# Kernel optimization log

Measured on AMD Instinct MI355X. Metric: run time of the kernel, lower is better.

Reference implementation:

```python
import jax, jax.numpy as jnp
import numpy as np

EMBED_DIM = 1024
NUM_HEADS = 16
HEAD_DIM = EMBED_DIM // NUM_HEADS
B, T = 8, 1024


def setup_inputs() -> dict:
    key = jax.random.key(0)
    ks = jax.random.split(key, 8)
    s = EMBED_DIM ** -0.5
    return {
        "query": jax.random.normal(ks[0], (B, T, EMBED_DIM), jnp.float32),
        "key": jax.random.normal(ks[1], (B, T, EMBED_DIM), jnp.float32),
        "value": jax.random.normal(ks[2], (B, T, EMBED_DIM), jnp.float32),
        "key_padding_mask": jnp.zeros((B, T), dtype=bool),
        "attn_mask": jax.random.normal(ks[3], (T, T), jnp.float32) * 0.02,
        "in_proj_weight": jax.random.normal(ks[4], (3 * EMBED_DIM, EMBED_DIM), jnp.float32) * s,
        "in_proj_bias": jax.random.normal(ks[5], (3 * EMBED_DIM,), jnp.float32) * 0.02,
        "out_proj_weight": jax.random.normal(ks[6], (EMBED_DIM, EMBED_DIM), jnp.float32) * s,
        "out_proj_bias": jax.random.normal(ks[7], (EMBED_DIM,), jnp.float32) * 0.02,
    }


def reference(query, key, value, key_padding_mask, attn_mask,
              in_proj_weight, in_proj_bias, out_proj_weight, out_proj_bias):
    E, H, Dh = EMBED_DIM, NUM_HEADS, HEAD_DIM
    scale = Dh ** -0.5
    w_q, w_k, w_v = in_proj_weight[:E], in_proj_weight[E:2 * E], in_proj_weight[2 * E:]
    b_q, b_k, b_v = in_proj_bias[:E], in_proj_bias[E:2 * E], in_proj_bias[2 * E:]

    b, t_q, _ = query.shape
    t_k = key.shape[1]
    # projections: F.linear(x, W, b) = x @ W.T + b
    q = (query @ w_q.T + b_q).reshape(b, t_q, H, Dh).transpose(0, 2, 1, 3)
    k = (key @ w_k.T + b_k).reshape(b, t_k, H, Dh).transpose(0, 2, 1, 3)
    v = (value @ w_v.T + b_v).reshape(b, t_k, H, Dh).transpose(0, 2, 1, 3)

    scores = jnp.einsum('bhqd,bhkd->bhqk', q, k) * scale  # [B,H,Tq,Tk]
    scores = jnp.where(key_padding_mask[:, None, None, :], -jnp.inf, scores)
    scores = scores + attn_mask  # broadcast [Tq,Tk] over batch/heads
    attn = jax.nn.softmax(scores, axis=-1)
    out = jnp.einsum('bhqk,bhkd->bhqd', attn, v)
    out = out.transpose(0, 2, 1, 3).reshape(b, t_q, E)
    return out @ out_proj_weight.T + out_proj_bias
```

## Files before the change

kernel.cpp:

```cpp
#include <hip/hip_runtime.h>
#include <cstdint>
#include <cstddef>

#define E_DIM   1024
#define NHEADS  16
#define DHEAD   64
#define BATCH   8
#define SEQ     1024
#define MROWS   (BATCH*SEQ)

#define LOG2E 1.44269504f

typedef __bf16 bf16;
typedef __attribute__((ext_vector_type(8))) __bf16 bf16x8;
typedef __attribute__((ext_vector_type(4))) __bf16 bf16x4;
typedef __attribute__((ext_vector_type(4))) float f32x4;

typedef const __attribute__((address_space(1))) unsigned int gu32;
typedef __attribute__((address_space(3))) unsigned int lu32;

__global__ __launch_bounds__(256)
void split_kernel(const float* __restrict__ src, bf16* __restrict__ hi,
                  bf16* __restrict__ lo, int n4)
{
    int i = blockIdx.x * 256 + threadIdx.x;
    if (i >= n4) return;
    float4 x = ((const float4*)src)[i];
    bf16x4 h, l;
    h[0] = (bf16)x.x; l[0] = (bf16)(x.x - (float)h[0]);
    h[1] = (bf16)x.y; l[1] = (bf16)(x.y - (float)h[1]);
    h[2] = (bf16)x.z; l[2] = (bf16)(x.z - (float)h[2]);
    h[3] = (bf16)x.w; l[3] = (bf16)(x.w - (float)h[3]);
    ((bf16x4*)hi)[i] = h;
    ((bf16x4*)lo)[i] = l;
}

__global__ __launch_bounds__(256)
void cvt_bf16_kernel(const float* __restrict__ src, bf16* __restrict__ dst,
                     float scale, int n4)
{
    int i = blockIdx.x * 256 + threadIdx.x;
    if (i >= n4) return;
    float4 x = ((const float4*)src)[i];
    bf16x4 h;
    h[0] = (bf16)(x.x * scale); h[1] = (bf16)(x.y * scale);
    h[2] = (bf16)(x.z * scale); h[3] = (bf16)(x.w * scale);
    ((bf16x4*)dst)[i] = h;
}

template<int AMODE>
__global__ __launch_bounds__(512, 2)
void gemm_nt_mfma(const float* __restrict__ Af0, const float* __restrict__ Af1,
                  const float* __restrict__ Af2,
                  const bf16* __restrict__ Ahi, const bf16* __restrict__ Alo,
                  const bf16* __restrict__ Whi, const bf16* __restrict__ Wlo,
                  const float* __restrict__ bias,
                  float* __restrict__ outF, bf16* __restrict__ outHi,
                  int M, int N, int K)
{
    __shared__ char  smemA[2][16384];
    __shared__ bf16  Whs[2][128 * 32];
    __shared__ bf16  Wls[2][128 * 32];

    const int tid  = threadIdx.x;
    const int lane = tid & 63;
    const int wid  = tid >> 6;
    const int wm = (wid >> 1) * 32;
    const int wn = (wid & 1) * 64;
    const int fr = lane & 15;
    const int fq = lane >> 4;
    const int fk = ((fq + (fr >> 1)) & 3) * 8;

    const int z = blockIdx.y;
    const float* Af = (z == 0) ? Af0 : (z == 1) ? Af1 : Af2;
    const bf16* Wh = Whi + (size_t)z * E_DIM * E_DIM;
    const bf16* Wl = Wlo + (size_t)z * E_DIM * E_DIM;
    const float* bs = bias + z * E_DIM;
    const int mode = AMODE ? ((z == 2) ? 2 : 1) : 0;

    const int id = blockIdx.x;
    const int mTile = (id & 7) + 8 * (id >> 6);
    const int nTile = (id >> 3) & 7;
    const int mBase = mTile * 128;
    const int nBase = nTile * 128;

    const int rowW  = tid >> 2;
    const int colW  = (((tid & 3) - ((tid >> 3) & 3)) & 3) * 8;
    const int rowAf  = tid >> 3;
    const int slotAf = ((tid & 7) - (rowAf & 7)) & 7;

    const int dcol = lane & 15;
    float bv[4];
#pragma unroll
    for (int bn = 0; bn < 4; ++bn)
        bv[bn] = bs[nBase + wn + bn * 16 + dcol];

    f32x4 acc[2][4];
#pragma unroll
    for (int i = 0; i < 2; ++i)
#pragma unroll
        for (int j = 0; j < 4; ++j) acc[i][j] = (f32x4){0.f, 0.f, 0.f, 0.f};

    const float* pAf0 = Af  + (size_t)(mBase + rowAf) * K + slotAf * 4;
    const float* pAf1 = pAf0 + (size_t)64 * K;
    const bf16*  pAh  = Ahi + (size_t)(mBase + rowW) * K + colW;
    const bf16*  pAl  = Alo + (size_t)(mBase + rowW) * K + colW;
    const bf16*  pWh  = Wh + (size_t)(nBase + rowW) * K + colW;
    const bf16*  pWl  = Wl + (size_t)(nBase + rowW) * K + colW;

    auto stage = [&](int bi) {
        if (AMODE == 1) {
            float* As = (float*)smemA[bi];
            __builtin_amdgcn_global_load_lds((gu32*)pAf0, (lu32*)&As[wid * 256],        16, 0, 0);
            __builtin_amdgcn_global_load_lds((gu32*)pAf1, (lu32*)&As[2048 + wid * 256], 16, 0, 0);
            pAf0 += 32; pAf1 += 32;
        } else {
            bf16* Ah = (bf16*)smemA[bi];
            bf16* Al = Ah + 4096;
            __builtin_amdgcn_global_load_lds((gu32*)pAh, (lu32*)&Ah[wid * 512], 16, 0, 0);
            __builtin_amdgcn_global_load_lds((gu32*)pAl, (lu32*)&Al[wid * 512], 16, 0, 0);
        }
        __builtin_amdgcn_global_load_lds((gu32*)pWh, (lu32*)&Whs[bi][wid * 512], 16, 0, 0);
        __builtin_amdgcn_global_load_lds((gu32*)pWl, (lu32*)&Wls[bi][wid * 512], 16, 0, 0);
        pAh += 32; pAl += 32; pWh += 32; pWl += 32;
    };

    stage(0);

    const int NIT = K >> 5;
#pragma unroll 1
    for (int it = 0; it < NIT; ++it) {
        const int cur = it & 1;
        if (it + 1 < NIT) {
            stage(cur ^ 1);
            asm volatile("s_waitcnt vmcnt(4)" ::: "memory");
        } else {
            asm volatile("s_waitcnt vmcnt(0)" ::: "memory");
        }
        __builtin_amdgcn_s_barrier();

        bf16x8 afh[2], afl[2], bfh[4], bfl[4];
        if (AMODE == 1) {
            const float* As = (const float*)smemA[cur];
#pragma unroll
            for (int am = 0; am < 2; ++am) {
                const int row = wm + am * 16 + fr;
                const float* Ar = &As[row * 32];
                f32x4 a0 = *(const f32x4*)&Ar[((2 * fq     + (fr & 7)) & 7) * 4];
                f32x4 a1 = *(const f32x4*)&Ar[((2 * fq + 1 + (fr & 7)) & 7) * 4];
                bf16x8 h, l;
#pragma unroll
                for (int j = 0; j < 4; ++j) {
                    h[j]     = (bf16)a0[j];
                    l[j]     = (bf16)(a0[j] - (float)h[j]);
                    h[j + 4] = (bf16)a1[j];
                    l[j + 4] = (bf16)(a1[j] - (float)h[j + 4]);
                }
                afh[am] = h; afl[am] = l;
            }
        } else {
            const bf16* Ah = (const bf16*)smemA[cur];
            const bf16* Al = Ah + 4096;
#pragma unroll
            for (int am = 0; am < 2; ++am) {
                afh[am] = *(const bf16x8*)&Ah[(wm + am * 16 + fr) * 32 + fk];
                afl[am] = *(const bf16x8*)&Al[(wm + am * 16 + fr) * 32 + fk];
            }
        }
#pragma unroll
        for (int bn = 0; bn < 4; ++bn) {
            bfh[bn] = *(const bf16x8*)&Whs[cur][(wn + bn * 16 + fr) * 32 + fk];
            bfl[bn] = *(const bf16x8*)&Wls[cur][(wn + bn * 16 + fr) * 32 + fk];
        }
        __builtin_amdgcn_s_setprio(1);
#pragma unroll
        for (int am = 0; am < 2; ++am)
#pragma unroll
            for (int bn = 0; bn < 4; ++bn) {
                acc[am][bn] = __builtin_amdgcn_mfma_f32_16x16x32_bf16(afh[am], bfh[bn], acc[am][bn], 0, 0, 0);
                acc[am][bn] = __builtin_amdgcn_mfma_f32_16x16x32_bf16(afh[am], bfl[bn], acc[am][bn], 0, 0, 0);
                acc[am][bn] = __builtin_amdgcn_mfma_f32_16x16x32_bf16(afl[am], bfh[bn], acc[am][bn], 0, 0, 0);
            }
        __builtin_amdgcn_s_setprio(0);
        __builtin_amdgcn_s_barrier();
    }

    const int drow = (lane >> 4) * 4;
#pragma unroll
    for (int bn = 0; bn < 4; ++bn) {
        const int col = nBase + wn + bn * 16 + dcol;
#pragma unroll
        for (int am = 0; am < 2; ++am) {
#pragma unroll
            for (int r = 0; r < 4; ++r) {
                const int row = mBase + wm + am * 16 + drow + r;
                const float v = acc[am][bn][r] + bv[bn];
                if (mode == 0) {
                    outF[(size_t)row * N + col] = v;
                } else {
                    const int b = row >> 10, t = row & 1023;
                    const int h = col >> 6,  d = col & 63;
                    size_t idx;
                    if (mode == 1)
                        idx = (((size_t)(b * NHEADS + h)) * SEQ + t) * DHEAD + d;
                    else
                        idx = (((size_t)(b * NHEADS + h)) * DHEAD + d) * SEQ + t;
                    outHi[(size_t)z * MROWS * E_DIM + idx] = (bf16)v;
                }
            }
        }
    }
}

__global__ __launch_bounds__(512)
void attn_mfma_kernel(const bf16* __restrict__ qkv,
                      const bf16* __restrict__ mask_bf,
                      const unsigned char* __restrict__ kpad,
                      bf16* __restrict__ ctx_hi, bf16* __restrict__ ctx_lo)
{
    __shared__ bf16 Ks [2][4096];
    __shared__ bf16 Vts[2][4096];
    __shared__ bf16 Pn[8][1024];

    const int tid  = threadIdx.x;
    const int lane = tid & 63;
    const int wid  = tid >> 6;
    const int c16  = lane & 15;
    const int quad = lane >> 4;

    const int bh = blockIdx.x;
    const int qt = blockIdx.y;
    const int b = bh >> 4, h = bh & 15;

    const size_t seg = (size_t)MROWS * E_DIM;
    const size_t headoff = (size_t)bh * SEQ * DHEAD;
    const bf16* Q_g  = qkv + headoff;
    const bf16* K_g  = qkv + seg + headoff;
    const bf16* Vt_g = qkv + 2 * seg + headoff;

    const int qglob = qt * 128 + wid * 16 + c16;

    bf16x8 qf[2];
#pragma unroll
    for (int ks = 0; ks < 2; ++ks)
        qf[ks] = *(const bf16x8*)&Q_g[(size_t)qglob * DHEAD + quad * 8 + ks * 32];

    float l_i = 0.f;
    f32x4 oacc[4];
#pragma unroll
    for (int dt = 0; dt < 4; ++dt) oacc[dt] = (f32x4){0.f, 0.f, 0.f, 0.f};

    const int row0 = tid >> 3;
    const int c0   = (tid & 7) ^ (row0 & 7);

    auto stage = [&](int kt, int bi) {
        const int ktb = kt * 64;
        const size_t k0 = (size_t)(ktb + row0) * DHEAD + c0 * 8;
        const size_t v0 = (size_t)row0 * SEQ + ktb + c0 * 8;
        __builtin_amdgcn_global_load_lds((gu32*)(K_g + k0),  (lu32*)&Ks [bi][wid * 512], 16, 0, 0);
        __builtin_amdgcn_global_load_lds((gu32*)(Vt_g + v0), (lu32*)&Vts[bi][wid * 512], 16, 0, 0);
    };

    stage(0, 0);
    __syncthreads();

    const int pxor = (c16 & 7) << 3;
    const size_t kpb = (size_t)b * SEQ + quad * 4;

#pragma unroll 1
    for (int kt = 0; kt < 16; ++kt) {
        const int cur = kt & 1;
        const int ktb = kt * 64;

        bf16x4 mvh[4];
        unsigned kpu[4];
#pragma unroll
        for (int st = 0; st < 4; ++st) {
            mvh[st] = *(const bf16x4*)&mask_bf[(size_t)qglob * SEQ + ktb + st * 16 + quad * 4];
            kpu[st] = *(const unsigned*)&kpad[kpb + ktb + st * 16];
        }

        if (kt < 15) stage(kt + 1, cur ^ 1);

        f32x4 sacc[4];
#pragma unroll
        for (int st = 0; st < 4; ++st) sacc[st] = (f32x4){0.f, 0.f, 0.f, 0.f};
        __builtin_amdgcn_s_setprio(1);
#pragma unroll
        for (int st = 0; st < 4; ++st) {
            const int row = st * 16 + c16;
            const int sw  = row & 7;
#pragma unroll
            for (int ks = 0; ks < 2; ++ks) {
                const int cp = ((quad + ks * 4) ^ sw);
                bf16x8 kh = *(const bf16x8*)&Ks[cur][(row * 8 + cp) * 8];
                sacc[st] = __builtin_amdgcn_mfma_f32_16x16x32_bf16(kh, qf[ks], sacc[st], 0, 0, 0);
            }
        }
        __builtin_amdgcn_s_setprio(0);

        float s[16];
#pragma unroll
        for (int st = 0; st < 4; ++st) {
#pragma unroll
            for (int r = 0; r < 4; ++r)
                s[st * 4 + r] = fmaf(sacc[st][r], 0.125f * LOG2E, (float)mvh[st][r]);
        }
        if (__any((kpu[0] | kpu[1] | kpu[2] | kpu[3]) != 0u)) {
#pragma unroll
            for (int st = 0; st < 4; ++st)
#pragma unroll
                for (int r = 0; r < 4; ++r)
                    if ((kpu[st] >> (r * 8)) & 0xff) s[st * 4 + r] = -2e30f;
        }
        float p[16];
#pragma unroll
        for (int i = 0; i < 16; ++i)
            p[i] = __builtin_amdgcn_exp2f(fminf(s[i], 30.f));
        float u8[8];
#pragma unroll
        for (int i = 0; i < 8; ++i) u8[i] = p[i] + p[i + 8];
#pragma unroll
        for (int i = 0; i < 4; ++i) u8[i] += u8[i + 4];
        float ps = (u8[0] + u8[1]) + (u8[2] + u8[3]);
        ps += __shfl_xor(ps, 16, 64);
        ps += __shfl_xor(ps, 32, 64);
        l_i += ps;

#pragma unroll
        for (int st = 0; st < 4; ++st) {
            bf16x4 ph;
#pragma unroll
            for (int r = 0; r < 4; ++r) ph[r] = (bf16)p[st * 4 + r];
            *(bf16x4*)&Pn[wid][c16 * 64 + ((st * 16 + quad * 4) ^ pxor)] = ph;
        }
        bf16x8 pf[2];
#pragma unroll
        for (int ks = 0; ks < 2; ++ks)
            pf[ks] = *(const bf16x8*)&Pn[wid][c16 * 64 + ((ks * 32 + quad * 8) ^ pxor)];

        __builtin_amdgcn_s_setprio(1);
#pragma unroll
        for (int dt = 0; dt < 4; ++dt) {
            const int row = dt * 16 + c16;
            const int sw  = row & 7;
#pragma unroll
            for (int ks = 0; ks < 2; ++ks) {
                const int cp = ((quad + ks * 4) ^ sw);
                bf16x8 vh = *(const bf16x8*)&Vts[cur][(row * 8 + cp) * 8];
                oacc[dt] = __builtin_amdgcn_mfma_f32_16x16x32_bf16(vh, pf[ks], oacc[dt], 0, 0, 0);
            }
        }
        __builtin_amdgcn_s_setprio(0);

        __syncthreads();
    }

    const float invl = 1.0f / l_i;
#pragma unroll
    for (int dt = 0; dt < 4; ++dt) {
        bf16x4 oh, ol;
#pragma unroll
        for (int r = 0; r < 4; ++r) {
            float v = oacc[dt][r] * invl;
            oh[r] = (bf16)v;
            ol[r] = (bf16)(v - (float)oh[r]);
        }
        size_t idx = ((size_t)b * SEQ + qglob) * E_DIM + h * DHEAD + dt * 16 + quad * 4;
        *(bf16x4*)&ctx_hi[idx] = oh;
        *(bf16x4*)&ctx_lo[idx] = ol;
    }
}

extern "C" void kernel_launch(void* const* d_in, const int* in_sizes, int n_in,
                              void* d_out, int out_size, void* d_ws, size_t ws_size,
                              hipStream_t stream)
{
    const float* q_in = (const float*)d_in[0];
    const float* k_in = (const float*)d_in[1];
    const float* v_in = (const float*)d_in[2];
    const unsigned char* kpad = (const unsigned char*)d_in[3];
    const float* attn_mask = (const float*)d_in[4];
    const float* w_in  = (const float*)d_in[5];
    const float* b_in  = (const float*)d_in[6];
    const float* w_out = (const float*)d_in[7];
    const float* b_out = (const float*)d_in[8];
    float* out = (float*)d_out;

    char* ws = (char*)d_ws;
    const size_t MB = 1024 * 1024;
    bf16* w_in_hi  = (bf16*)(ws + 0 * MB);
    bf16* w_in_lo  = (bf16*)(ws + 6 * MB);
    bf16* w_out_hi = (bf16*)(ws + 12 * MB);
    bf16* w_out_lo = (bf16*)(ws + 14 * MB);
    bf16* qkv      = (bf16*)(ws + 16 * MB);
    bf16* mask_bf  = (bf16*)(ws + 64 * MB);
    bf16* ctx_hi   = (bf16*)(ws + 66 * MB);
    bf16* ctx_lo   = (bf16*)(ws + 82 * MB);

    split_kernel<<<(3 * E_DIM * E_DIM / 4 + 255) / 256, 256, 0, stream>>>(
        w_in, w_in_hi, w_in_lo, 3 * E_DIM * E_DIM / 4);
    split_kernel<<<(E_DIM * E_DIM / 4 + 255) / 256, 256, 0, stream>>>(
        w_out, w_out_hi, w_out_lo, E_DIM * E_DIM / 4);
    cvt_bf16_kernel<<<(SEQ * SEQ / 4 + 255) / 256, 256, 0, stream>>>(
        attn_mask, mask_bf, LOG2E, SEQ * SEQ / 4);

    gemm_nt_mfma<1><<<dim3(512, 3), 512, 0, stream>>>(
        q_in, k_in, v_in,
        nullptr, nullptr,
        w_in_hi, w_in_lo, b_in,
        nullptr, qkv,
        MROWS, E_DIM, E_DIM);

    attn_mfma_kernel<<<dim3(BATCH * NHEADS, SEQ / 128), 512, 0, stream>>>(
        qkv, mask_bf, kpad, ctx_hi, ctx_lo);

    gemm_nt_mfma<0><<<dim3(512, 1), 512, 0, stream>>>(
        nullptr, nullptr, nullptr,
        ctx_hi, ctx_lo, w_out_hi, w_out_lo, b_out,
        out, nullptr,
        MROWS, E_DIM, E_DIM);
}
```

Baseline: 446.5 us.

## Halve GEMM block threads with 64x64 warp tiles and single-barrier prefetch

Both projection GEMMs now run with 256 threads per block instead of 512. Each wave computes a 64x64 output tile instead of 32x64, so every loaded B fragment is reused across more MFMAs, and each thread issues more global-to-LDS loads per stage. The K loop now uses one __syncthreads at the top, reads fragments into registers, then prefetches the next buffer before the MFMAs, replacing the explicit vmcnt waits and second barrier. This trades fewer waves per CU and higher register pressure for better register-level reuse and less barrier overhead. Correctness relies on __syncthreads waiting for the outstanding async LDS loads.

```diff
diff --git a/kernel.cpp b/kernel.cpp
--- a/kernel.cpp
+++ b/kernel.cpp
@@ -49,7 +49,7 @@
 }
 
 template<int AMODE>
-__global__ __launch_bounds__(512, 2)
+__global__ __launch_bounds__(256, 2)
 void gemm_nt_mfma(const float* __restrict__ Af0, const float* __restrict__ Af1,
                   const float* __restrict__ Af2,
                   const bf16* __restrict__ Ahi, const bf16* __restrict__ Alo,
@@ -65,7 +65,7 @@
     const int tid  = threadIdx.x;
     const int lane = tid & 63;
     const int wid  = tid >> 6;
-    const int wm = (wid >> 1) * 32;
+    const int wm = (wid >> 1) * 64;
     const int wn = (wid & 1) * 64;
     const int fr = lane & 15;
     const int fq = lane >> 4;
@@ -95,34 +95,46 @@
     for (int bn = 0; bn < 4; ++bn)
         bv[bn] = bs[nBase + wn + bn * 16 + dcol];
 
-    f32x4 acc[2][4];
-#pragma unroll
-    for (int i = 0; i < 2; ++i)
+    f32x4 acc[4][4];
+#pragma unroll
+    for (int i = 0; i < 4; ++i)
 #pragma unroll
         for (int j = 0; j < 4; ++j) acc[i][j] = (f32x4){0.f, 0.f, 0.f, 0.f};
 
-    const float* pAf0 = Af  + (size_t)(mBase + rowAf) * K + slotAf * 4;
-    const float* pAf1 = pAf0 + (size_t)64 * K;
-    const bf16*  pAh  = Ahi + (size_t)(mBase + rowW) * K + colW;
-    const bf16*  pAl  = Alo + (size_t)(mBase + rowW) * K + colW;
-    const bf16*  pWh  = Wh + (size_t)(nBase + rowW) * K + colW;
-    const bf16*  pWl  = Wl + (size_t)(nBase + rowW) * K + colW;
+    const float* pAf = Af  + (size_t)(mBase + rowAf) * K + slotAf * 4;
+    const bf16*  pAh = Ahi + (size_t)(mBase + rowW) * K + colW;
+    const bf16*  pAl = Alo + (size_t)(mBase + rowW) * K + colW;
+    const bf16*  pWh = Wh  + (size_t)(nBase + rowW) * K + colW;
+    const bf16*  pWl = Wl  + (size_t)(nBase + rowW) * K + colW;
 
     auto stage = [&](int bi) {
         if (AMODE == 1) {
             float* As = (float*)smemA[bi];
-            __builtin_amdgcn_global_load_lds((gu32*)pAf0, (lu32*)&As[wid * 256],        16, 0, 0);
-            __builtin_amdgcn_global_load_lds((gu32*)pAf1, (lu32*)&As[2048 + wid * 256], 16, 0, 0);
-            pAf0 += 32; pAf1 += 32;
+#pragma unroll
+            for (int i = 0; i < 4; ++i)
+                __builtin_amdgcn_global_load_lds((gu32*)(pAf + (size_t)(i * 32) * K),
+                                                 (lu32*)&As[i * 1024 + wid * 256], 16, 0, 0);
+            pAf += 32;
         } else {
             bf16* Ah = (bf16*)smemA[bi];
             bf16* Al = Ah + 4096;
-            __builtin_amdgcn_global_load_lds((gu32*)pAh, (lu32*)&Ah[wid * 512], 16, 0, 0);
-            __builtin_amdgcn_global_load_lds((gu32*)pAl, (lu32*)&Al[wid * 512], 16, 0, 0);
-        }
-        __builtin_amdgcn_global_load_lds((gu32*)pWh, (lu32*)&Whs[bi][wid * 512], 16, 0, 0);
-        __builtin_amdgcn_global_load_lds((gu32*)pWl, (lu32*)&Wls[bi][wid * 512], 16, 0, 0);
-        pAh += 32; pAl += 32; pWh += 32; pWl += 32;
+#pragma unroll
+            for (int j = 0; j < 2; ++j) {
+                __builtin_amdgcn_global_load_lds((gu32*)(pAh + (size_t)(j * 64) * K),
+                                                 (lu32*)&Ah[j * 2048 + wid * 512], 16, 0, 0);
+                __builtin_amdgcn_global_load_lds((gu32*)(pAl + (size_t)(j * 64) * K),
+                                                 (lu32*)&Al[j * 2048 + wid * 512], 16, 0, 0);
+            }
+            pAh += 32; pAl += 32;
+        }
+#pragma unroll
+        for (int j = 0; j < 2; ++j) {
+            __builtin_amdgcn_global_load_lds((gu32*)(pWh + (size_t)(j * 64) * K),
+                                             (lu32*)&Whs[bi][j * 2048 + wid * 512], 16, 0, 0);
+            __builtin_amdgcn_global_load_lds((gu32*)(pWl + (size_t)(j * 64) * K),
+                                             (lu32*)&Wls[bi][j * 2048 + wid * 512], 16, 0, 0);
+        }
+        pWh += 32; pWl += 32;
     };
 
     stage(0);
@@ -131,19 +143,13 @@
 #pragma unroll 1
     for (int it = 0; it < NIT; ++it) {
         const int cur = it & 1;
-        if (it + 1 < NIT) {
-            stage(cur ^ 1);
-            asm volatile("s_waitcnt vmcnt(4)" ::: "memory");
-        } else {
-            asm volatile("s_waitcnt vmcnt(0)" ::: "memory");
-        }
-        __builtin_amdgcn_s_barrier();
-
-        bf16x8 afh[2], afl[2], bfh[4], bfl[4];
+        __syncthreads();
+
+        bf16x8 afh[4], afl[4], bfh[4], bfl[4];
         if (AMODE == 1) {
             const float* As = (const float*)smemA[cur];
 #pragma unroll
-            for (int am = 0; am < 2; ++am) {
+            for (int am = 0; am < 4; ++am) {
                 const int row = wm + am * 16 + fr;
                 const float* Ar = &As[row * 32];
                 f32x4 a0 = *(const f32x4*)&Ar[((2 * fq     + (fr & 7)) & 7) * 4];
@@ -162,7 +168,7 @@
             const bf16* Ah = (const bf16*)smemA[cur];
             const bf16* Al = Ah + 4096;
 #pragma unroll
-            for (int am = 0; am < 2; ++am) {
+            for (int am = 0; am < 4; ++am) {
                 afh[am] = *(const bf16x8*)&Ah[(wm + am * 16 + fr) * 32 + fk];
                 afl[am] = *(const bf16x8*)&Al[(wm + am * 16 + fr) * 32 + fk];
             }
@@ -172,9 +178,12 @@
             bfh[bn] = *(const bf16x8*)&Whs[cur][(wn + bn * 16 + fr) * 32 + fk];
             bfl[bn] = *(const bf16x8*)&Wls[cur][(wn + bn * 16 + fr) * 32 + fk];
         }
+
+        if (it + 1 < NIT) stage(cur ^ 1);
+
         __builtin_amdgcn_s_setprio(1);
 #pragma unroll
-        for (int am = 0; am < 2; ++am)
+        for (int am = 0; am < 4; ++am)
 #pragma unroll
             for (int bn = 0; bn < 4; ++bn) {
                 acc[am][bn] = __builtin_amdgcn_mfma_f32_16x16x32_bf16(afh[am], bfh[bn], acc[am][bn], 0, 0, 0);
@@ -182,7 +191,6 @@
                 acc[am][bn] = __builtin_amdgcn_mfma_f32_16x16x32_bf16(afl[am], bfh[bn], acc[am][bn], 0, 0, 0);
             }
         __builtin_amdgcn_s_setprio(0);
-        __builtin_amdgcn_s_barrier();
     }
 
     const int drow = (lane >> 4) * 4;
@@ -190,7 +198,7 @@
     for (int bn = 0; bn < 4; ++bn) {
         const int col = nBase + wn + bn * 16 + dcol;
 #pragma unroll
-        for (int am = 0; am < 2; ++am) {
+        for (int am = 0; am < 4; ++am) {
 #pragma unroll
             for (int r = 0; r < 4; ++r) {
                 const int row = mBase + wm + am * 16 + drow + r;
@@ -405,7 +413,7 @@
     cvt_bf16_kernel<<<(SEQ * SEQ / 4 + 255) / 256, 256, 0, stream>>>(
         attn_mask, mask_bf, LOG2E, SEQ * SEQ / 4);
 
-    gemm_nt_mfma<1><<<dim3(512, 3), 512, 0, stream>>>(
+    gemm_nt_mfma<1><<<dim3(512, 3), 256, 0, stream>>>(
         q_in, k_in, v_in,
         nullptr, nullptr,
         w_in_hi, w_in_lo, b_in,
@@ -415,7 +423,7 @@
     attn_mfma_kernel<<<dim3(BATCH * NHEADS, SEQ / 128), 512, 0, stream>>>(
         qkv, mask_bf, kpad, ctx_hi, ctx_lo);
 
-    gemm_nt_mfma<0><<<dim3(512, 1), 512, 0, stream>>>(
+    gemm_nt_mfma<0><<<dim3(512, 1), 256, 0, stream>>>(
         nullptr, nullptr, nullptr,
         ctx_hi, ctx_lo, w_out_hi, w_out_lo, b_out,
         out, nullptr,
```

New measurement: 451.7 us. About the same (+1.2%).
